# Kernel tuning notes

Measured on AMD Instinct MI355X. Metric: run time of the kernel, lower is better.

## Reference

```python
import jax, jax.numpy as jnp
import numpy as np

MOMENTUM = 0.9
SHRINK = 0.0025
EPS_ATTN = 1e-8
EPS_NORM = 1e-12


def setup_inputs() -> dict:
    key = jax.random.key(0)
    ks = jax.random.split(key, 6)
    N, L, C, M = 64, 2048, 256, 128
    query = jax.random.normal(ks[0], (N, L, C), dtype=jnp.float32)
    mem = jax.random.normal(ks[1], (M, C), dtype=jnp.float32)
    # mimic xavier_normal + L2 row-normalize init
    mem = mem * np.sqrt(2.0 / (M + C))
    mem = mem / jnp.maximum(jnp.linalg.norm(mem, axis=1, keepdims=True), EPS_NORM)
    scale = 1.0 / np.sqrt(C)
    U_w = jax.random.uniform(ks[2], (C, C), jnp.float32, -scale, scale)
    U_b = jax.random.uniform(ks[3], (C,), jnp.float32, -scale, scale)
    W_w = jax.random.uniform(ks[4], (C, C), jnp.float32, -scale, scale)
    W_b = jax.random.uniform(ks[5], (C,), jnp.float32, -scale, scale)
    return {"query": query, "mem": mem, "U_w": U_w, "U_b": U_b, "W_w": W_w, "W_b": W_b}


def _hard_shrink_relu(x, lambd=SHRINK, epsilon=EPS_NORM):
    d = x - lambd
    return jax.nn.relu(d) * x / (jnp.abs(d) + epsilon)


def reference(query, mem, U_w, U_b, W_w, W_b):
    N, L, C = query.shape
    M = mem.shape[0]
    q = query.reshape(-1, C)  # T x C

    # ---- update (torch.no_grad block) ----
    qd = jax.lax.stop_gradient(q)
    m = jax.lax.stop_gradient(mem)
    attn_u = jax.nn.softmax(qd @ m.T, axis=-1)          # T x M
    attn_u = jnp.maximum(attn_u, EPS_ATTN)
    add_mem = attn_u.T @ qd                              # M x C
    gate = jax.nn.sigmoid(m @ U_w.T + U_b + add_mem @ W_w.T + W_b)
    new_mem = MOMENTUM * m + (1.0 - MOMENTUM) * ((1.0 - gate) * m + gate * add_mem)
    new_mem = new_mem / jnp.maximum(jnp.linalg.norm(new_mem, axis=1, keepdims=True), EPS_NORM)
    new_mem = jax.lax.stop_gradient(new_mem)

    # ---- read (memory detached, query differentiable) ----
    attn = jax.nn.softmax(q @ new_mem.T, axis=-1)        # T x M
    attn = _hard_shrink_relu(attn)
    attn = attn / jnp.maximum(jnp.sum(jnp.abs(attn), axis=1, keepdims=True), EPS_NORM)
    add_memory = attn @ new_mem                          # T x C
    out = jnp.concatenate([q, add_memory], axis=1)       # T x 2C

    out = out.reshape(N, L, 2 * C)
    attn = attn.reshape(N, L, M)
    return out, attn, new_mem
```

## Files before the change

kernel.cpp:

```cpp
#include <hip/hip_runtime.h>
#include <hip/hip_bf16.h>

#define T_TOT 131072

typedef __bf16 v8bf __attribute__((ext_vector_type(8)));
typedef float  v4f  __attribute__((ext_vector_type(4)));

#define MFMA16(a, b, c) __builtin_amdgcn_mfma_f32_16x16x32_bf16(a, b, c, 0, 0, 0)

__device__ __forceinline__ unsigned short f2bf(float x) {
  unsigned int u = __float_as_uint(x);
  u += 0x7fffu + ((u >> 16) & 1u);
  return (unsigned short)(u >> 16);
}
__device__ __forceinline__ ushort4 f2bf4(float4 v) {
  ushort4 r; r.x = f2bf(v.x); r.y = f2bf(v.y); r.z = f2bf(v.z); r.w = f2bf(v.w);
  return r;
}

__global__ void prep_kernel(const float* __restrict__ mem,
                            unsigned short* __restrict__ memb,
                            float* __restrict__ add_mem) {
  int i = blockIdx.x * 256 + threadIdx.x;
  memb[i] = f2bf(mem[i]);
  add_mem[i] = 0.f;
}

template <bool IS_READ>
__global__ __launch_bounds__(256, 2)
void attn_kernel(const float* __restrict__ q,
                 const unsigned short* __restrict__ memb,
                 unsigned short* __restrict__ attnT,
                 float* __restrict__ attn_out,
                 const unsigned short* __restrict__ nmT,
                 float* __restrict__ out) {
  constexpr int R1 = 33792;
  __shared__ __align__(16) char smem[IS_READ ? (R1 + 17408) : R1];
  unsigned short* qs   = (unsigned short*)smem;
  unsigned short* ms   = (unsigned short*)(smem + 9216);
  float*          S    = (float*)smem;
  unsigned short* nmTl = (unsigned short*)smem;
  unsigned short* P    = (unsigned short*)(smem + R1);

  const int tid  = threadIdx.x;
  const int wave = tid >> 6, lane = tid & 63, l15 = lane & 15, quad = lane >> 4;
  const int t0 = blockIdx.x * 64;
  const int rh = wave >> 1, mh = wave & 1;

  v4f acc[2][4] = {};

  for (int kc = 0; kc < 256; kc += 64) {
    __syncthreads();
#pragma unroll
    for (int i = 0; i < 4; ++i) {
      int f4 = tid + i * 256, row = f4 >> 4, c4 = f4 & 15;
      float4 v = *(const float4*)(q + (size_t)(t0 + row) * 256 + kc + c4 * 4);
      if constexpr (IS_READ)
        *(float4*)(out + (size_t)(t0 + row) * 512 + kc + c4 * 4) = v;
      *(ushort4*)(qs + row * 72 + c4 * 4) = f2bf4(v);
    }
#pragma unroll
    for (int i = 0; i < 4; ++i) {
      int g = tid + i * 256, m = g >> 3, c8 = g & 7;
      *(uint4*)(ms + m * 72 + c8 * 8) = *(const uint4*)(memb + m * 256 + kc + c8 * 8);
    }
    __syncthreads();
#pragma unroll
    for (int s = 0; s < 2; ++s) {
      int ko = s * 32 + quad * 8;
      v8bf a0 = *(const v8bf*)(qs + (rh * 32 + l15) * 72 + ko);
      v8bf a1 = *(const v8bf*)(qs + (rh * 32 + 16 + l15) * 72 + ko);
#pragma unroll
      for (int j = 0; j < 4; ++j) {
        v8bf b = *(const v8bf*)(ms + (mh * 64 + j * 16 + l15) * 72 + ko);
        acc[0][j] = MFMA16(a0, b, acc[0][j]);
        acc[1][j] = MFMA16(a1, b, acc[1][j]);
      }
    }
  }
  __syncthreads();
#pragma unroll
  for (int i = 0; i < 2; ++i)
#pragma unroll
    for (int j = 0; j < 4; ++j)
#pragma unroll
      for (int r = 0; r < 4; ++r)
        S[(rh * 32 + i * 16 + quad * 4 + r) * 132 + mh * 64 + j * 16 + l15] = acc[i][j][r];
  __syncthreads();

  const int row = tid >> 2, p = tid & 3;
  float4 v[8];
  float mx = -1e30f;
#pragma unroll
  for (int k = 0; k < 8; ++k) {
    v[k] = *(const float4*)(S + row * 132 + p * 32 + k * 4);
    mx = fmaxf(mx, fmaxf(fmaxf(v[k].x, v[k].y), fmaxf(v[k].z, v[k].w)));
  }
  mx = fmaxf(mx, __shfl_xor(mx, 1, 64));
  mx = fmaxf(mx, __shfl_xor(mx, 2, 64));
  float sum = 0.f;
#pragma unroll
  for (int k = 0; k < 8; ++k) {
    v[k].x = __expf(v[k].x - mx); v[k].y = __expf(v[k].y - mx);
    v[k].z = __expf(v[k].z - mx); v[k].w = __expf(v[k].w - mx);
    sum += v[k].x + v[k].y + v[k].z + v[k].w;
  }
  sum += __shfl_xor(sum, 1, 64);
  sum += __shfl_xor(sum, 2, 64);
  float inv = 1.f / sum;

  if constexpr (!IS_READ) {
#pragma unroll
    for (int k = 0; k < 8; ++k) {
      v[k].x = fmaxf(v[k].x * inv, 1e-8f); v[k].y = fmaxf(v[k].y * inv, 1e-8f);
      v[k].z = fmaxf(v[k].z * inv, 1e-8f); v[k].w = fmaxf(v[k].w * inv, 1e-8f);
      *(float4*)(S + row * 132 + p * 32 + k * 4) = v[k];
    }
    __syncthreads();
    int m = tid >> 1, hf = tid & 1;
    unsigned int pk[16];
#pragma unroll
    for (int k2 = 0; k2 < 16; ++k2) {
      unsigned int lo = f2bf(S[(hf * 32 + k2 * 2) * 132 + m]);
      unsigned int hi = f2bf(S[(hf * 32 + k2 * 2 + 1) * 132 + m]);
      pk[k2] = lo | (hi << 16);
    }
    uint4* dst = (uint4*)(attnT + (size_t)m * T_TOT + t0 + hf * 32);
    dst[0] = make_uint4(pk[0], pk[1], pk[2], pk[3]);
    dst[1] = make_uint4(pk[4], pk[5], pk[6], pk[7]);
    dst[2] = make_uint4(pk[8], pk[9], pk[10], pk[11]);
    dst[3] = make_uint4(pk[12], pk[13], pk[14], pk[15]);
  } else {
    float ysum = 0.f;
#pragma unroll
    for (int k = 0; k < 8; ++k) {
      float* e = (float*)&v[k];
#pragma unroll
      for (int c = 0; c < 4; ++c) {
        float a2 = e[c] * inv;
        float dd = a2 - 0.0025f;
        float y  = dd > 0.f ? a2 * dd / (dd + 1e-12f) : 0.f;
        e[c] = y; ysum += y;
      }
    }
    ysum += __shfl_xor(ysum, 1, 64);
    ysum += __shfl_xor(ysum, 2, 64);
    float dn = 1.f / fmaxf(ysum, 1e-12f);
#pragma unroll
    for (int k = 0; k < 8; ++k) {
      float4 w; w.x = v[k].x * dn; w.y = v[k].y * dn; w.z = v[k].z * dn; w.w = v[k].w * dn;
      *(float4*)(attn_out + (size_t)(t0 + row) * 128 + p * 32 + k * 4) = w;
      *(ushort4*)(P + row * 136 + p * 32 + k * 4) = f2bf4(w);
    }
    __syncthreads();

    v4f acc2[16] = {};
    for (int mc = 0; mc < 128; mc += 32) {
#pragma unroll
      for (int i = 0; i < 4; ++i) {
        int g = tid + i * 256, cr = g >> 2, c8 = g & 3;
        *(uint4*)(nmTl + cr * 56 + c8 * 8) = *(const uint4*)(nmT + cr * 128 + mc + c8 * 8);
      }
      __syncthreads();
      v8bf af = *(const v8bf*)(P + (wave * 16 + l15) * 136 + mc + quad * 8);
#pragma unroll
      for (int j2 = 0; j2 < 16; ++j2) {
        v8bf bf = *(const v8bf*)(nmTl + (j2 * 16 + l15) * 56 + quad * 8);
        acc2[j2] = MFMA16(af, bf, acc2[j2]);
      }
      __syncthreads();
    }
#pragma unroll
    for (int j2 = 0; j2 < 16; ++j2)
#pragma unroll
      for (int r = 0; r < 4; ++r)
        out[(size_t)(t0 + wave * 16 + quad * 4 + r) * 512 + 256 + j2 * 16 + l15] = acc2[j2][r];
  }
}

__global__ __launch_bounds__(256, 2)
void addmem_kernel(const unsigned short* __restrict__ attnT,
                   const float* __restrict__ q,
                   float* __restrict__ add_mem) {
  __shared__ __align__(16) char smem[18432 + 22528];
  unsigned short* at_l = (unsigned short*)smem;
  unsigned short* qT_l = (unsigned short*)(smem + 18432);
  const int tid  = threadIdx.x;
  const int wave = tid >> 6, lane = tid & 63, l15 = lane & 15, quad = lane >> 4;
  const int h  = blockIdx.x & 1;
  const int tc = blockIdx.x >> 1;
  const int wm = wave & 1, wc = wave >> 1;
  v4f acc[4][4] = {};

  for (int kk = 0; kk < 8; ++kk) {
    int kb = tc * 512 + kk * 64;
    __syncthreads();
#pragma unroll
    for (int i = 0; i < 4; ++i) {
      int g = tid + i * 256, m = g >> 3, t8 = g & 7;
      *(uint4*)(at_l + m * 72 + t8 * 8) =
          *(const uint4*)(attnT + (size_t)m * T_TOT + kb + t8 * 8);
    }
    {
      int tr = tid >> 2, cg = tid & 3;
#pragma unroll
      for (int f = 0; f < 8; ++f) {
        float4 vq = *(const float4*)(q + (size_t)(kb + tr) * 256 + h * 128 + f * 16 + cg * 4);
        int cb = f * 16 + cg * 4;
        qT_l[(cb + 0) * 88 + tr] = f2bf(vq.x);
        qT_l[(cb + 1) * 88 + tr] = f2bf(vq.y);
        qT_l[(cb + 2) * 88 + tr] = f2bf(vq.z);
        qT_l[(cb + 3) * 88 + tr] = f2bf(vq.w);
      }
    }
    __syncthreads();
#pragma unroll
    for (int s = 0; s < 2; ++s) {
      int ko = s * 32 + quad * 8;
      v8bf a[4], b[4];
#pragma unroll
      for (int jm = 0; jm < 4; ++jm)
        a[jm] = *(const v8bf*)(at_l + (wm * 64 + jm * 16 + l15) * 72 + ko);
#pragma unroll
      for (int jc = 0; jc < 4; ++jc)
        b[jc] = *(const v8bf*)(qT_l + (wc * 64 + jc * 16 + l15) * 88 + ko);
#pragma unroll
      for (int jm = 0; jm < 4; ++jm)
#pragma unroll
        for (int jc = 0; jc < 4; ++jc)
          acc[jm][jc] = MFMA16(a[jm], b[jc], acc[jm][jc]);
    }
  }
#pragma unroll
  for (int jm = 0; jm < 4; ++jm)
#pragma unroll
    for (int jc = 0; jc < 4; ++jc)
#pragma unroll
      for (int r = 0; r < 4; ++r)
        atomicAdd(add_mem + (wm * 64 + jm * 16 + quad * 4 + r) * 256 +
                      h * 128 + wc * 64 + jc * 16 + l15,
                  acc[jm][jc][r]);
}

__global__ __launch_bounds__(256)
void update_kernel(const float* __restrict__ mem, const float* __restrict__ add_mem,
                   const float* __restrict__ U_w, const float* __restrict__ U_b,
                   const float* __restrict__ W_w, const float* __restrict__ W_b,
                   float* __restrict__ nm_out, unsigned short* __restrict__ nm_bf,
                   unsigned short* __restrict__ nmT_bf) {
  const int m = blockIdx.x, c = threadIdx.x;
  __shared__ float mrow[256], arow[256], red[8];
  mrow[c] = mem[m * 256 + c];
  arow[c] = add_mem[m * 256 + c];
  __syncthreads();
  float g = U_b[c] + W_b[c];
  const float4* uw = (const float4*)(U_w + (size_t)c * 256);
  const float4* ww = (const float4*)(W_w + (size_t)c * 256);
#pragma unroll 8
  for (int k = 0; k < 64; ++k) {
    float4 u4 = uw[k], w4 = ww[k];
    g += u4.x * mrow[k * 4] + u4.y * mrow[k * 4 + 1] + u4.z * mrow[k * 4 + 2] + u4.w * mrow[k * 4 + 3];
    g += w4.x * arow[k * 4] + w4.y * arow[k * 4 + 1] + w4.z * arow[k * 4 + 2] + w4.w * arow[k * 4 + 3];
  }
  float gate = 1.f / (1.f + __expf(-g));
  float nmv = mrow[c] * (1.f - 0.1f * gate) + 0.1f * gate * arow[c];
  float ss = nmv * nmv;
#pragma unroll
  for (int o = 1; o < 64; o <<= 1) ss += __shfl_xor(ss, o, 64);
  int wv = c >> 6, lane = c & 63;
  if (lane == 0) red[wv] = ss;
  __syncthreads();
  if (c == 0) red[4] = 1.f / fmaxf(sqrtf(red[0] + red[1] + red[2] + red[3]), 1e-12f);
  __syncthreads();
  float nv = nmv * red[4];
  nm_out[m * 256 + c] = nv;
  unsigned short b = f2bf(nv);
  nm_bf[m * 256 + c] = b;
  nmT_bf[c * 128 + m] = b;
}

extern "C" void kernel_launch(void* const* d_in, const int* in_sizes, int n_in,
                              void* d_out, int out_size, void* d_ws, size_t ws_size,
                              hipStream_t stream) {
  (void)in_sizes; (void)n_in; (void)out_size; (void)ws_size;
  const float* q   = (const float*)d_in[0];
  const float* mem = (const float*)d_in[1];
  const float* U_w = (const float*)d_in[2];
  const float* U_b = (const float*)d_in[3];
  const float* W_w = (const float*)d_in[4];
  const float* W_b = (const float*)d_in[5];

  float* out      = (float*)d_out;
  float* attn_out = out + (size_t)T_TOT * 512;
  float* nm_out   = attn_out + (size_t)T_TOT * 128;

  float*          add_mem = (float*)d_ws;
  unsigned short* mem_bf  = (unsigned short*)((char*)d_ws + 131072);
  unsigned short* nm_bf   = (unsigned short*)((char*)d_ws + 196608);
  unsigned short* nmT_bf  = (unsigned short*)((char*)d_ws + 262144);
  unsigned short* attnT = (unsigned short*)attn_out;

  prep_kernel<<<128, 256, 0, stream>>>(mem, mem_bf, add_mem);
  attn_kernel<false><<<2048, 256, 0, stream>>>(q, mem_bf, attnT, nullptr, nullptr, nullptr);
  addmem_kernel<<<512, 256, 0, stream>>>(attnT, q, add_mem);
  update_kernel<<<128, 256, 0, stream>>>(mem, add_mem, U_w, U_b, W_w, W_b,
                                         nm_out, nm_bf, nmT_bf);
  attn_kernel<true><<<2048, 256, 0, stream>>>(q, nm_bf, nullptr, attn_out, nmT_bf, out);
}
```

Measured before the change: 579.7 us.

## Emit transposed bf16 query in attn pass and stream GEMM operands from global

```diff
diff --git a/kernel.cpp b/kernel.cpp
--- a/kernel.cpp
+++ b/kernel.cpp
@@ -27,58 +27,48 @@
 }
 
 template <bool IS_READ>
-__global__ __launch_bounds__(256, 2)
+__global__ __launch_bounds__(256, IS_READ ? 3 : 2)
 void attn_kernel(const float* __restrict__ q,
                  const unsigned short* __restrict__ memb,
                  unsigned short* __restrict__ attnT,
+                 unsigned short* __restrict__ qbT,
                  float* __restrict__ attn_out,
                  const unsigned short* __restrict__ nmT,
                  float* __restrict__ out) {
-  constexpr int R1 = 33792;
-  __shared__ __align__(16) char smem[IS_READ ? (R1 + 17408) : R1];
-  unsigned short* qs   = (unsigned short*)smem;
-  unsigned short* ms   = (unsigned short*)(smem + 9216);
-  float*          S    = (float*)smem;
-  unsigned short* nmTl = (unsigned short*)smem;
-  unsigned short* P    = (unsigned short*)(smem + R1);
+  __shared__ __align__(16) char smem[IS_READ ? 51200 : 67584];
+  unsigned short* qs = (unsigned short*)smem;
+  float*          S  = (float*)(IS_READ ? smem : (smem + 33792));
+  unsigned short* P  = (unsigned short*)(smem + 33792);
 
   const int tid  = threadIdx.x;
   const int wave = tid >> 6, lane = tid & 63, l15 = lane & 15, quad = lane >> 4;
   const int t0 = blockIdx.x * 64;
   const int rh = wave >> 1, mh = wave & 1;
 
+#pragma unroll
+  for (int i = 0; i < 16; ++i) {
+    int f4 = tid + i * 256, row = f4 >> 6, c4 = f4 & 63;
+    float4 v = *(const float4*)(q + (size_t)(t0 + row) * 256 + c4 * 4);
+    if constexpr (IS_READ)
+      *(float4*)(out + (size_t)(t0 + row) * 512 + c4 * 4) = v;
+    *(ushort4*)(qs + row * 264 + c4 * 4) = f2bf4(v);
+  }
+  __syncthreads();
+
   v4f acc[2][4] = {};
-
-  for (int kc = 0; kc < 256; kc += 64) {
-    __syncthreads();
-#pragma unroll
-    for (int i = 0; i < 4; ++i) {
-      int f4 = tid + i * 256, row = f4 >> 4, c4 = f4 & 15;
-      float4 v = *(const float4*)(q + (size_t)(t0 + row) * 256 + kc + c4 * 4);
-      if constexpr (IS_READ)
-        *(float4*)(out + (size_t)(t0 + row) * 512 + kc + c4 * 4) = v;
-      *(ushort4*)(qs + row * 72 + c4 * 4) = f2bf4(v);
-    }
-#pragma unroll
-    for (int i = 0; i < 4; ++i) {
-      int g = tid + i * 256, m = g >> 3, c8 = g & 7;
-      *(uint4*)(ms + m * 72 + c8 * 8) = *(const uint4*)(memb + m * 256 + kc + c8 * 8);
-    }
-    __syncthreads();
-#pragma unroll
-    for (int s = 0; s < 2; ++s) {
-      int ko = s * 32 + quad * 8;
-      v8bf a0 = *(const v8bf*)(qs + (rh * 32 + l15) * 72 + ko);
-      v8bf a1 = *(const v8bf*)(qs + (rh * 32 + 16 + l15) * 72 + ko);
-#pragma unroll
-      for (int j = 0; j < 4; ++j) {
-        v8bf b = *(const v8bf*)(ms + (mh * 64 + j * 16 + l15) * 72 + ko);
-        acc[0][j] = MFMA16(a0, b, acc[0][j]);
-        acc[1][j] = MFMA16(a1, b, acc[1][j]);
-      }
-    }
-  }
-  __syncthreads();
+#pragma unroll
+  for (int ks = 0; ks < 8; ++ks) {
+    int ko = ks * 32 + quad * 8;
+    v8bf a0 = *(const v8bf*)(qs + (rh * 32 + l15) * 264 + ko);
+    v8bf a1 = *(const v8bf*)(qs + (rh * 32 + 16 + l15) * 264 + ko);
+#pragma unroll
+    for (int j = 0; j < 4; ++j) {
+      v8bf b = *(const v8bf*)(memb + (size_t)(mh * 64 + j * 16 + l15) * 256 + ko);
+      acc[0][j] = MFMA16(a0, b, acc[0][j]);
+      acc[1][j] = MFMA16(a1, b, acc[1][j]);
+    }
+  }
+  if constexpr (IS_READ) __syncthreads();
 #pragma unroll
   for (int i = 0; i < 2; ++i)
 #pragma unroll
@@ -117,19 +107,38 @@
       *(float4*)(S + row * 132 + p * 32 + k * 4) = v[k];
     }
     __syncthreads();
-    int m = tid >> 1, hf = tid & 1;
-    unsigned int pk[16];
-#pragma unroll
-    for (int k2 = 0; k2 < 16; ++k2) {
-      unsigned int lo = f2bf(S[(hf * 32 + k2 * 2) * 132 + m]);
-      unsigned int hi = f2bf(S[(hf * 32 + k2 * 2 + 1) * 132 + m]);
-      pk[k2] = lo | (hi << 16);
-    }
-    uint4* dst = (uint4*)(attnT + (size_t)m * T_TOT + t0 + hf * 32);
-    dst[0] = make_uint4(pk[0], pk[1], pk[2], pk[3]);
-    dst[1] = make_uint4(pk[4], pk[5], pk[6], pk[7]);
-    dst[2] = make_uint4(pk[8], pk[9], pk[10], pk[11]);
-    dst[3] = make_uint4(pk[12], pk[13], pk[14], pk[15]);
+    {
+      int m = tid >> 1, hf = tid & 1;
+      unsigned int pk[16];
+#pragma unroll
+      for (int k2 = 0; k2 < 16; ++k2) {
+        unsigned int lo = f2bf(S[(hf * 32 + k2 * 2) * 132 + m]);
+        unsigned int hi = f2bf(S[(hf * 32 + k2 * 2 + 1) * 132 + m]);
+        pk[k2] = lo | (hi << 16);
+      }
+      uint4* dst = (uint4*)(attnT + (size_t)m * T_TOT + t0 + hf * 32);
+      dst[0] = make_uint4(pk[0], pk[1], pk[2], pk[3]);
+      dst[1] = make_uint4(pk[4], pk[5], pk[6], pk[7]);
+      dst[2] = make_uint4(pk[8], pk[9], pk[10], pk[11]);
+      dst[3] = make_uint4(pk[12], pk[13], pk[14], pk[15]);
+    }
+    {
+      const int c = tid;
+      const unsigned short* qcol = qs + c;
+      uint4* dq = (uint4*)(qbT + (size_t)c * T_TOT + t0);
+#pragma unroll
+      for (int g = 0; g < 4; ++g) {
+        unsigned int pk2[8];
+#pragma unroll
+        for (int t2 = 0; t2 < 8; ++t2) {
+          unsigned int lo = qcol[(g * 16 + t2 * 2) * 264];
+          unsigned int hi = qcol[(g * 16 + t2 * 2 + 1) * 264];
+          pk2[t2] = lo | (hi << 16);
+        }
+        dq[g * 2]     = make_uint4(pk2[0], pk2[1], pk2[2], pk2[3]);
+        dq[g * 2 + 1] = make_uint4(pk2[4], pk2[5], pk2[6], pk2[7]);
+      }
+    }
   } else {
     float ysum = 0.f;
 #pragma unroll
@@ -155,20 +164,14 @@
     __syncthreads();
 
     v4f acc2[16] = {};
+#pragma unroll
     for (int mc = 0; mc < 128; mc += 32) {
-#pragma unroll
-      for (int i = 0; i < 4; ++i) {
-        int g = tid + i * 256, cr = g >> 2, c8 = g & 3;
-        *(uint4*)(nmTl + cr * 56 + c8 * 8) = *(const uint4*)(nmT + cr * 128 + mc + c8 * 8);
-      }
-      __syncthreads();
       v8bf af = *(const v8bf*)(P + (wave * 16 + l15) * 136 + mc + quad * 8);
 #pragma unroll
       for (int j2 = 0; j2 < 16; ++j2) {
-        v8bf bf = *(const v8bf*)(nmTl + (j2 * 16 + l15) * 56 + quad * 8);
+        v8bf bf = *(const v8bf*)(nmT + (size_t)(j2 * 16 + l15) * 128 + mc + quad * 8);
         acc2[j2] = MFMA16(af, bf, acc2[j2]);
       }
-      __syncthreads();
     }
 #pragma unroll
     for (int j2 = 0; j2 < 16; ++j2)
@@ -180,56 +183,34 @@
 
 __global__ __launch_bounds__(256, 2)
 void addmem_kernel(const unsigned short* __restrict__ attnT,
-                   const float* __restrict__ q,
+                   const unsigned short* __restrict__ qbT,
                    float* __restrict__ add_mem) {
-  __shared__ __align__(16) char smem[18432 + 22528];
-  unsigned short* at_l = (unsigned short*)smem;
-  unsigned short* qT_l = (unsigned short*)(smem + 18432);
   const int tid  = threadIdx.x;
   const int wave = tid >> 6, lane = tid & 63, l15 = lane & 15, quad = lane >> 4;
-  const int h  = blockIdx.x & 1;
-  const int tc = blockIdx.x >> 1;
+  const int lb = ((blockIdx.x & 7) << 6) | (blockIdx.x >> 3);
+  const int h  = lb & 1;
+  const int tc = lb >> 1;
   const int wm = wave & 1, wc = wave >> 1;
   v4f acc[4][4] = {};
 
-  for (int kk = 0; kk < 8; ++kk) {
-    int kb = tc * 512 + kk * 64;
-    __syncthreads();
-#pragma unroll
-    for (int i = 0; i < 4; ++i) {
-      int g = tid + i * 256, m = g >> 3, t8 = g & 7;
-      *(uint4*)(at_l + m * 72 + t8 * 8) =
-          *(const uint4*)(attnT + (size_t)m * T_TOT + kb + t8 * 8);
-    }
-    {
-      int tr = tid >> 2, cg = tid & 3;
-#pragma unroll
-      for (int f = 0; f < 8; ++f) {
-        float4 vq = *(const float4*)(q + (size_t)(kb + tr) * 256 + h * 128 + f * 16 + cg * 4);
-        int cb = f * 16 + cg * 4;
-        qT_l[(cb + 0) * 88 + tr] = f2bf(vq.x);
-        qT_l[(cb + 1) * 88 + tr] = f2bf(vq.y);
-        qT_l[(cb + 2) * 88 + tr] = f2bf(vq.z);
-        qT_l[(cb + 3) * 88 + tr] = f2bf(vq.w);
-      }
-    }
-    __syncthreads();
-#pragma unroll
-    for (int s = 0; s < 2; ++s) {
-      int ko = s * 32 + quad * 8;
-      v8bf a[4], b[4];
-#pragma unroll
-      for (int jm = 0; jm < 4; ++jm)
-        a[jm] = *(const v8bf*)(at_l + (wm * 64 + jm * 16 + l15) * 72 + ko);
+  const unsigned short* aBase = attnT + (size_t)(wm * 64 + l15) * T_TOT + tc * 512 + quad * 8;
+  const unsigned short* bBase = qbT + (size_t)(h * 128 + wc * 64 + l15) * T_TOT + tc * 512 + quad * 8;
+
+#pragma unroll 2
+  for (int kk = 0; kk < 16; ++kk) {
+    int ko = kk * 32;
+    v8bf a[4], b[4];
+#pragma unroll
+    for (int jm = 0; jm < 4; ++jm)
+      a[jm] = *(const v8bf*)(aBase + (size_t)jm * 16 * T_TOT + ko);
+#pragma unroll
+    for (int jc = 0; jc < 4; ++jc)
+      b[jc] = *(const v8bf*)(bBase + (size_t)jc * 16 * T_TOT + ko);
+#pragma unroll
+    for (int jm = 0; jm < 4; ++jm)
 #pragma unroll
       for (int jc = 0; jc < 4; ++jc)
-        b[jc] = *(const v8bf*)(qT_l + (wc * 64 + jc * 16 + l15) * 88 + ko);
-#pragma unroll
-      for (int jm = 0; jm < 4; ++jm)
-#pragma unroll
-        for (int jc = 0; jc < 4; ++jc)
-          acc[jm][jc] = MFMA16(a[jm], b[jc], acc[jm][jc]);
-    }
+        acc[jm][jc] = MFMA16(a[jm], b[jc], acc[jm][jc]);
   }
 #pragma unroll
   for (int jm = 0; jm < 4; ++jm)
@@ -299,11 +280,12 @@
   unsigned short* nm_bf   = (unsigned short*)((char*)d_ws + 196608);
   unsigned short* nmT_bf  = (unsigned short*)((char*)d_ws + 262144);
   unsigned short* attnT = (unsigned short*)attn_out;
+  unsigned short* qbT   = (unsigned short*)out;
 
   prep_kernel<<<128, 256, 0, stream>>>(mem, mem_bf, add_mem);
-  attn_kernel<false><<<2048, 256, 0, stream>>>(q, mem_bf, attnT, nullptr, nullptr, nullptr);
-  addmem_kernel<<<512, 256, 0, stream>>>(attnT, q, add_mem);
+  attn_kernel<false><<<2048, 256, 0, stream>>>(q, mem_bf, attnT, qbT, nullptr, nullptr, nullptr);
+  addmem_kernel<<<512, 256, 0, stream>>>(attnT, qbT, add_mem);
   update_kernel<<<128, 256, 0, stream>>>(mem, add_mem, U_w, U_b, W_w, W_b,
                                          nm_out, nm_bf, nmT_bf);
-  attn_kernel<true><<<2048, 256, 0, stream>>>(q, nm_bf, nullptr, attn_out, nmT_bf, out);
-}
+  attn_kernel<true><<<2048, 256, 0, stream>>>(q, nm_bf, nullptr, nullptr, attn_out, nmT_bf, out);
+}
```

After: 676.7 us. 1.17x slower.
